# Performance work log

Measured on AMD Instinct MI355X. Metric: run time of the kernel, lower is better.

Reference implementation:

```python
import jax, jax.numpy as jnp
import numpy as np

EPS = 0.001

def _conv1x1(h, w, b):
    # h: [n,c,v,w_dim], w: [o,c], b: [o]  -> [n,o,v,w_dim]
    return jnp.einsum('ncvw,oc->novw', h, w) + b[None, :, None, None]

def setup_inputs() -> dict:
    key = jax.random.key(0)
    ks = jax.random.split(key, 10)
    N, Cin, T, V = 16, 64, 64, 384
    inp = {
        'x': jax.random.normal(ks[0], (N, Cin, T, V), dtype=jnp.float32),
        'A': jax.random.uniform(ks[1], (N, 8, V, V), dtype=jnp.float32),
        'conv_w': jax.random.normal(ks[2], (64, Cin), dtype=jnp.float32) * 0.05,
        'conv_b': jax.random.normal(ks[3], (64,), dtype=jnp.float32) * 0.05,
        'w1': jax.random.normal(ks[4], (16, 7), dtype=jnp.float32) * 0.2,
        'b1': jax.random.normal(ks[5], (16,), dtype=jnp.float32) * 0.05,
        'w2': jax.random.normal(ks[6], (32, 16), dtype=jnp.float32) * 0.2,
        'b2': jax.random.normal(ks[7], (32,), dtype=jnp.float32) * 0.05,
        'w3': jax.random.normal(ks[8], (64, 32), dtype=jnp.float32) * 0.2,
        'b3': jax.random.normal(ks[9], (64,), dtype=jnp.float32) * 0.05,
    }
    return inp

def reference(x, A, conv_w, conv_b, w1, b1, w2, b2, w3, b3):
    # self.conv: 1x1 conv (t_kernel_size=1) mapping in_channels -> out_channels*kernel_size = 64
    x = jnp.einsum('nctv,oc->notv', x, conv_w) + conv_b[None, :, None, None]
    mask = A[:, 7][:, None]              # [n,1,v,w]
    h = A[:, :7]                         # [n,7,v,w]
    # adjmatder: three 1x1 convs with ReLU (dropout = identity in eval mode)
    h = jax.nn.relu(_conv1x1(h, w1, b1))
    h = jax.nn.relu(_conv1x1(h, w2, b2))
    h = jax.nn.relu(_conv1x1(h, w3, b3))   # [n,64,v,w]
    Am = h * mask
    Dl = 1.0 / (Am.sum(axis=2) + EPS)      # degree-inverse over v: [n,64,w]
    An = Am * Dl[:, :, None, :]            # einsum 'ncvw,ncw->ncvw'
    out = jnp.einsum('nctv,ncvw->nctw', x, An)
    return out, An
```

## Files before the change

### kernel.cpp

```cpp
#include <hip/hip_runtime.h>

#define EPS_F 0.001f

constexpr int Nn = 16;
constexpr int Cc = 64;
constexpr int Tt = 64;
constexpr int Vv = 384;
constexpr size_t TV = (size_t)Tt * Vv;
constexpr size_t VW = (size_t)Vv * Vv;
constexpr size_t OUT0 = (size_t)Nn * Cc * TV;

__global__ __launch_bounds__(256) void k_conv(const float* __restrict__ x,
        const float* __restrict__ cw, const float* __restrict__ cb,
        float* __restrict__ xc) {
    __shared__ float wt[64 * 64];
    const int tid = threadIdx.x;
    for (int i = tid; i < 4096; i += 256) {
        int o = i & 63, c = i >> 6;
        wt[c * 64 + o] = cw[o * 64 + c];
    }
    __syncthreads();
    const int b = blockIdx.x;
    const int n = b / 48;
    const int pos = (b % 48) * 512 + tid;
    const float* xin = x + (size_t)n * Cc * TV + pos;
    float acc0[64], acc1[64];
#pragma unroll
    for (int o = 0; o < 64; ++o) { acc0[o] = 0.f; acc1[o] = 0.f; }
    for (int c = 0; c < 64; ++c) {
        float x0 = xin[(size_t)c * TV];
        float x1 = xin[(size_t)c * TV + 256];
        const float4* wr = (const float4*)(wt + c * 64);
#pragma unroll
        for (int oq = 0; oq < 16; ++oq) {
            float4 w4 = wr[oq];
            acc0[oq*4+0] += x0 * w4.x; acc0[oq*4+1] += x0 * w4.y;
            acc0[oq*4+2] += x0 * w4.z; acc0[oq*4+3] += x0 * w4.w;
            acc1[oq*4+0] += x1 * w4.x; acc1[oq*4+1] += x1 * w4.y;
            acc1[oq*4+2] += x1 * w4.z; acc1[oq*4+3] += x1 * w4.w;
        }
    }
    float* xo = xc + (size_t)n * Cc * TV + pos;
#pragma unroll
    for (int o = 0; o < 64; ++o) {
        float bo = cb[o];
        xo[(size_t)o * TV]       = acc0[o] + bo;
        xo[(size_t)o * TV + 256] = acc1[o] + bo;
    }
}

__global__ __launch_bounds__(384) void k_am(const float* __restrict__ A,
        const float* __restrict__ w1, const float* __restrict__ b1,
        const float* __restrict__ w2, const float* __restrict__ b2,
        const float* __restrict__ w3, const float* __restrict__ b3,
        float* __restrict__ Am) {
    __shared__ __align__(16) float sw1[16 * 8];
    __shared__ __align__(16) float sw2[32 * 16];
    __shared__ __align__(16) float sw3[64 * 32];
    __shared__ float sb1[16], sb2[32], sb3[64];
    const int tid = threadIdx.x;
    if (tid < 128) {
        int o = tid >> 3, k = tid & 7;
        sw1[tid] = (k < 7) ? w1[o * 7 + k] : 0.f;
    }
    for (int i = tid; i < 512; i += 384)  sw2[i] = w2[i];
    for (int i = tid; i < 2048; i += 384) sw3[i] = w3[i];
    if (tid < 16) sb1[tid] = b1[tid];
    else if (tid < 48) sb2[tid - 16] = b2[tid - 16];
    else if (tid < 112) sb3[tid - 48] = b3[tid - 48];
    __syncthreads();

    const int b = blockIdx.x;
    const int n = b / 192;
    const int v0 = (b % 192) * 2;
    const float* Ab = A + (size_t)n * 8 * VW + (size_t)v0 * Vv + tid;
    float aA[8], aB[8];
#pragma unroll
    for (int k = 0; k < 8; ++k) {
        aA[k] = Ab[(size_t)k * VW];
        aB[k] = Ab[(size_t)k * VW + Vv];
    }
    float h1A[16], h1B[16];
#pragma unroll
    for (int o = 0; o < 16; ++o) {
        float4 wa = *(const float4*)(sw1 + o * 8);
        float4 wb = *(const float4*)(sw1 + o * 8 + 4);
        float tA = sb1[o], tB = sb1[o];
        tA += wa.x*aA[0] + wa.y*aA[1] + wa.z*aA[2] + wa.w*aA[3];
        tA += wb.x*aA[4] + wb.y*aA[5] + wb.z*aA[6] + wb.w*aA[7];
        tB += wa.x*aB[0] + wa.y*aB[1] + wa.z*aB[2] + wa.w*aB[3];
        tB += wb.x*aB[4] + wb.y*aB[5] + wb.z*aB[6] + wb.w*aB[7];
        h1A[o] = fmaxf(tA, 0.f);
        h1B[o] = fmaxf(tB, 0.f);
    }
    float h2A[32], h2B[32];
#pragma unroll
    for (int o = 0; o < 32; ++o) {
        const float4* wr = (const float4*)(sw2 + o * 16);
        float tA = sb2[o], tB = sb2[o];
#pragma unroll
        for (int q = 0; q < 4; ++q) {
            float4 w4 = wr[q];
            tA += w4.x*h1A[q*4+0] + w4.y*h1A[q*4+1] + w4.z*h1A[q*4+2] + w4.w*h1A[q*4+3];
            tB += w4.x*h1B[q*4+0] + w4.y*h1B[q*4+1] + w4.z*h1B[q*4+2] + w4.w*h1B[q*4+3];
        }
        h2A[o] = fmaxf(tA, 0.f);
        h2B[o] = fmaxf(tB, 0.f);
    }
    const float mA = aA[7], mB = aB[7];
    float* apA = Am + (size_t)n * 64 * VW + (size_t)v0 * Vv + tid;
#pragma unroll
    for (int o = 0; o < 64; ++o) {
        const float4* wr = (const float4*)(sw3 + o * 32);
        float tA = sb3[o], tB = sb3[o];
#pragma unroll
        for (int q = 0; q < 8; ++q) {
            float4 w4 = wr[q];
            tA += w4.x*h2A[q*4+0] + w4.y*h2A[q*4+1] + w4.z*h2A[q*4+2] + w4.w*h2A[q*4+3];
            tB += w4.x*h2B[q*4+0] + w4.y*h2B[q*4+1] + w4.z*h2B[q*4+2] + w4.w*h2B[q*4+3];
        }
        apA[(size_t)o * VW]      = fmaxf(tA, 0.f) * mA;
        apA[(size_t)o * VW + Vv] = fmaxf(tB, 0.f) * mB;
    }
}

__global__ __launch_bounds__(256) void k_gemm(const float* __restrict__ xc,
        float* __restrict__ An, float* __restrict__ out) {
    __shared__ float As[16 * 68];
    __shared__ float Bs[16 * 68];
    __shared__ float4 part[256];
    __shared__ __align__(16) float dlr[64];
    const int tid = threadIdx.x;
    const int bid = blockIdx.x;
    const int b = (bid & 7) * 768 + (bid >> 3);
    const int batch = b / 6;
    const int w0 = (b % 6) * 64;
    const float* Ap = xc + (size_t)batch * TV;
    float* Bp = An + (size_t)batch * VW + w0;
    const int ty = tid / 16, tx = tid % 16;
    const int lr = tid / 4,  lq = tid % 4;
    const int br = tid / 16, bc = tid % 16;
    float acc[4][4];
#pragma unroll
    for (int i = 0; i < 4; ++i)
#pragma unroll
        for (int j = 0; j < 4; ++j) acc[i][j] = 0.f;
    float4 cs = make_float4(0.f, 0.f, 0.f, 0.f);
    float4 a4 = *(const float4*)(Ap + (size_t)lr * 384 + lq * 4);
    float4 b4 = *(const float4*)(Bp + (size_t)br * 384 + bc * 4);
    for (int k0 = 0; k0 < 384; k0 += 16) {
        cs.x += b4.x; cs.y += b4.y; cs.z += b4.z; cs.w += b4.w;
        As[(lq*4+0)*68 + lr] = a4.x;
        As[(lq*4+1)*68 + lr] = a4.y;
        As[(lq*4+2)*68 + lr] = a4.z;
        As[(lq*4+3)*68 + lr] = a4.w;
        *(float4*)(Bs + br * 68 + bc * 4) = b4;
        __syncthreads();
        if (k0 + 16 < 384) {
            a4 = *(const float4*)(Ap + (size_t)lr * 384 + (k0 + 16) + lq * 4);
            b4 = *(const float4*)(Bp + (size_t)(k0 + 16 + br) * 384 + bc * 4);
        }
#pragma unroll
        for (int kk = 0; kk < 16; ++kk) {
            float4 av = *(const float4*)(As + kk * 68 + ty * 4);
            float4 bv = *(const float4*)(Bs + kk * 68 + tx * 4);
            float aa[4] = {av.x, av.y, av.z, av.w};
            float bb[4] = {bv.x, bv.y, bv.z, bv.w};
#pragma unroll
            for (int i = 0; i < 4; ++i)
#pragma unroll
                for (int j = 0; j < 4; ++j) acc[i][j] += aa[i] * bb[j];
        }
        __syncthreads();
    }
    part[tid] = cs;
    __syncthreads();
    if (tid < 64) {
        const int q = tid >> 2, e = tid & 3;
        float s = 0.f;
#pragma unroll
        for (int r = 0; r < 16; ++r) {
            const float* p4 = (const float*)&part[r * 16 + q];
            s += p4[e];
        }
        dlr[tid] = 1.f / (s + EPS_F);
    }
    __syncthreads();
    const float4 d4 = *(const float4*)(dlr + tx * 4);
    for (int k0 = 0; k0 < 384; k0 += 16) {
        float* bp = Bp + (size_t)(k0 + br) * 384 + bc * 4;
        float4 v = *(const float4*)bp;
        v.x *= d4.x; v.y *= d4.y; v.z *= d4.z; v.w *= d4.w;
        *(float4*)bp = v;
    }
    float* op = out + (size_t)batch * TV + w0 + tx * 4;
#pragma unroll
    for (int i = 0; i < 4; ++i) {
        float4 o4 = make_float4(acc[i][0] * d4.x, acc[i][1] * d4.y,
                                acc[i][2] * d4.z, acc[i][3] * d4.w);
        *(float4*)(op + (size_t)(ty * 4 + i) * 384) = o4;
    }
}

extern "C" void kernel_launch(void* const* d_in, const int* in_sizes, int n_in,
                              void* d_out, int out_size, void* d_ws, size_t ws_size,
                              hipStream_t stream) {
    const float* x  = (const float*)d_in[0];
    const float* A  = (const float*)d_in[1];
    const float* cw = (const float*)d_in[2];
    const float* cb = (const float*)d_in[3];
    const float* w1 = (const float*)d_in[4];
    const float* b1 = (const float*)d_in[5];
    const float* w2 = (const float*)d_in[6];
    const float* b2 = (const float*)d_in[7];
    const float* w3 = (const float*)d_in[8];
    const float* b3 = (const float*)d_in[9];

    float* out = (float*)d_out;
    float* An  = out + OUT0;
    float* xc  = (float*)d_ws;

    k_conv<<<768, 256, 0, stream>>>(x, cw, cb, xc);
    k_am  <<<3072, 384, 0, stream>>>(A, w1, b1, w2, b2, w3, b3, An);
    k_gemm<<<6144, 256, 0, stream>>>(xc, An, out);
}
```

Baseline: 1.404 ms.

## Run batched GEMM as single-wavefront blocks with 8x8 register tiles

The batched x·An GEMM now runs one 64-thread wavefront per block instead of 256 threads. Each thread computes an 8x8 output microtile from 4 staged float4 loads per operand, which gives more FMAs per LDS read. Block-wide __syncthreads are replaced by s_waitcnt and a sched_barrier, and the column-sum reduction becomes wave shuffles instead of an LDS partial buffer. In exchange, the kernel uses more registers per thread, and correctness relies on in-order LDS access within a single wavefront.

Measured after the change: 1.354 ms. 3.6% less time.

```diff
diff --git a/kernel.cpp b/kernel.cpp
--- a/kernel.cpp
+++ b/kernel.cpp
@@ -124,11 +124,10 @@
     }
 }
 
-__global__ __launch_bounds__(256) void k_gemm(const float* __restrict__ xc,
+__global__ __launch_bounds__(64) void k_gemm(const float* __restrict__ xc,
         float* __restrict__ An, float* __restrict__ out) {
-    __shared__ float As[16 * 68];
-    __shared__ float Bs[16 * 68];
-    __shared__ float4 part[256];
+    __shared__ float As[16][68];
+    __shared__ float Bs[16][68];
     __shared__ __align__(16) float dlr[64];
     const int tid = threadIdx.x;
     const int bid = blockIdx.x;
@@ -137,68 +136,90 @@
     const int w0 = (b % 6) * 64;
     const float* Ap = xc + (size_t)batch * TV;
     float* Bp = An + (size_t)batch * VW + w0;
-    const int ty = tid / 16, tx = tid % 16;
-    const int lr = tid / 4,  lq = tid % 4;
-    const int br = tid / 16, bc = tid % 16;
-    float acc[4][4];
-#pragma unroll
-    for (int i = 0; i < 4; ++i)
-#pragma unroll
-        for (int j = 0; j < 4; ++j) acc[i][j] = 0.f;
+
+    const int lq = tid & 3,  lr4 = tid >> 2;
+    const int c4 = tid & 15, rg  = tid >> 4;
+    const int tx = tid & 7,  ty  = tid >> 3;
+
+    float4 ap[4], bp[4];
+#pragma unroll
+    for (int i = 0; i < 4; ++i) {
+        ap[i] = *(const float4*)(Ap + (size_t)(lr4 * 4 + i) * 384 + lq * 4);
+        bp[i] = *(const float4*)(Bp + (size_t)(rg * 4 + i) * 384 + c4 * 4);
+    }
     float4 cs = make_float4(0.f, 0.f, 0.f, 0.f);
-    float4 a4 = *(const float4*)(Ap + (size_t)lr * 384 + lq * 4);
-    float4 b4 = *(const float4*)(Bp + (size_t)br * 384 + bc * 4);
+    float acc[8][8];
+#pragma unroll
+    for (int i = 0; i < 8; ++i)
+#pragma unroll
+        for (int j = 0; j < 8; ++j) acc[i][j] = 0.f;
+
     for (int k0 = 0; k0 < 384; k0 += 16) {
-        cs.x += b4.x; cs.y += b4.y; cs.z += b4.z; cs.w += b4.w;
-        As[(lq*4+0)*68 + lr] = a4.x;
-        As[(lq*4+1)*68 + lr] = a4.y;
-        As[(lq*4+2)*68 + lr] = a4.z;
-        As[(lq*4+3)*68 + lr] = a4.w;
-        *(float4*)(Bs + br * 68 + bc * 4) = b4;
-        __syncthreads();
+#pragma unroll
+        for (int i = 0; i < 4; ++i) {
+            As[lq*4+0][lr4*4+i] = ap[i].x;
+            As[lq*4+1][lr4*4+i] = ap[i].y;
+            As[lq*4+2][lr4*4+i] = ap[i].z;
+            As[lq*4+3][lr4*4+i] = ap[i].w;
+            *(float4*)&Bs[rg*4+i][c4*4] = bp[i];
+            cs.x += bp[i].x; cs.y += bp[i].y; cs.z += bp[i].z; cs.w += bp[i].w;
+        }
+        asm volatile("s_waitcnt lgkmcnt(0)" ::: "memory");
+        __builtin_amdgcn_sched_barrier(0);
         if (k0 + 16 < 384) {
-            a4 = *(const float4*)(Ap + (size_t)lr * 384 + (k0 + 16) + lq * 4);
-            b4 = *(const float4*)(Bp + (size_t)(k0 + 16 + br) * 384 + bc * 4);
+#pragma unroll
+            for (int i = 0; i < 4; ++i) {
+                ap[i] = *(const float4*)(Ap + (size_t)(lr4*4+i) * 384 + (k0+16) + lq*4);
+                bp[i] = *(const float4*)(Bp + (size_t)(k0+16 + rg*4+i) * 384 + c4*4);
+            }
         }
 #pragma unroll
         for (int kk = 0; kk < 16; ++kk) {
-            float4 av = *(const float4*)(As + kk * 68 + ty * 4);
-            float4 bv = *(const float4*)(Bs + kk * 68 + tx * 4);
-            float aa[4] = {av.x, av.y, av.z, av.w};
-            float bb[4] = {bv.x, bv.y, bv.z, bv.w};
-#pragma unroll
-            for (int i = 0; i < 4; ++i)
-#pragma unroll
-                for (int j = 0; j < 4; ++j) acc[i][j] += aa[i] * bb[j];
-        }
-        __syncthreads();
-    }
-    part[tid] = cs;
-    __syncthreads();
-    if (tid < 64) {
-        const int q = tid >> 2, e = tid & 3;
-        float s = 0.f;
-#pragma unroll
-        for (int r = 0; r < 16; ++r) {
-            const float* p4 = (const float*)&part[r * 16 + q];
-            s += p4[e];
-        }
-        dlr[tid] = 1.f / (s + EPS_F);
-    }
-    __syncthreads();
-    const float4 d4 = *(const float4*)(dlr + tx * 4);
-    for (int k0 = 0; k0 < 384; k0 += 16) {
-        float* bp = Bp + (size_t)(k0 + br) * 384 + bc * 4;
-        float4 v = *(const float4*)bp;
-        v.x *= d4.x; v.y *= d4.y; v.z *= d4.z; v.w *= d4.w;
-        *(float4*)bp = v;
-    }
-    float* op = out + (size_t)batch * TV + w0 + tx * 4;
-#pragma unroll
-    for (int i = 0; i < 4; ++i) {
-        float4 o4 = make_float4(acc[i][0] * d4.x, acc[i][1] * d4.y,
-                                acc[i][2] * d4.z, acc[i][3] * d4.w);
-        *(float4*)(op + (size_t)(ty * 4 + i) * 384) = o4;
+            float4 a0 = *(const float4*)&As[kk][ty*8];
+            float4 a1 = *(const float4*)&As[kk][ty*8+4];
+            float4 b0 = *(const float4*)&Bs[kk][tx*4];
+            float4 b1 = *(const float4*)&Bs[kk][tx*4+32];
+            float av[8] = {a0.x,a0.y,a0.z,a0.w,a1.x,a1.y,a1.z,a1.w};
+            float bv[8] = {b0.x,b0.y,b0.z,b0.w,b1.x,b1.y,b1.z,b1.w};
+#pragma unroll
+            for (int i = 0; i < 8; ++i)
+#pragma unroll
+                for (int j = 0; j < 8; ++j) acc[i][j] += av[i] * bv[j];
+        }
+    }
+    cs.x += __shfl_xor(cs.x, 16); cs.y += __shfl_xor(cs.y, 16);
+    cs.z += __shfl_xor(cs.z, 16); cs.w += __shfl_xor(cs.w, 16);
+    cs.x += __shfl_xor(cs.x, 32); cs.y += __shfl_xor(cs.y, 32);
+    cs.z += __shfl_xor(cs.z, 32); cs.w += __shfl_xor(cs.w, 32);
+    if (tid < 16) {
+        float4 r;
+        r.x = 1.f / (cs.x + EPS_F); r.y = 1.f / (cs.y + EPS_F);
+        r.z = 1.f / (cs.z + EPS_F); r.w = 1.f / (cs.w + EPS_F);
+        *(float4*)&dlr[tid * 4] = r;
+    }
+    asm volatile("s_waitcnt lgkmcnt(0)" ::: "memory");
+    {
+        const float4 dc = *(const float4*)&dlr[c4 * 4];
+        float* sp = Bp + (size_t)rg * 384 + c4 * 4;
+#pragma unroll 4
+        for (int it = 0; it < 96; ++it) {
+            float4 v = *(const float4*)sp;
+            v.x *= dc.x; v.y *= dc.y; v.z *= dc.z; v.w *= dc.w;
+            *(float4*)sp = v;
+            sp += 4 * 384;
+        }
+    }
+    const float4 da = *(const float4*)&dlr[tx * 4];
+    const float4 db = *(const float4*)&dlr[tx * 4 + 32];
+    float* op = out + (size_t)batch * TV + w0;
+#pragma unroll
+    for (int i = 0; i < 8; ++i) {
+        float4 o0 = make_float4(acc[i][0]*da.x, acc[i][1]*da.y,
+                                acc[i][2]*da.z, acc[i][3]*da.w);
+        float4 o1 = make_float4(acc[i][4]*db.x, acc[i][5]*db.y,
+                                acc[i][6]*db.z, acc[i][7]*db.w);
+        *(float4*)(op + (size_t)(ty*8+i) * 384 + tx*4)      = o0;
+        *(float4*)(op + (size_t)(ty*8+i) * 384 + tx*4 + 32) = o1;
     }
 }
 
@@ -222,5 +243,5 @@
 
     k_conv<<<768, 256, 0, stream>>>(x, cw, cb, xc);
     k_am  <<<3072, 384, 0, stream>>>(A, w1, b1, w2, b2, w3, b3, An);
-    k_gemm<<<6144, 256, 0, stream>>>(xc, An, out);
-}
+    k_gemm<<<6144, 64, 0, stream>>>(xc, An, out);
+}
```
